# Kernel tuning notes

Measured on AMD Instinct MI355X. Metric: run time of the kernel, lower is better.

Reference implementation:

```python
import jax, jax.numpy as jnp
import numpy as np

B, N, DIN, DOUT = 2048, 64, 512, 512


def setup_inputs() -> dict:
    key = jax.random.key(0)
    kx, kw, kb = jax.random.split(key, 3)
    x = jax.random.normal(kx, (B, N, DIN), dtype=jnp.float32)
    # stacked per-node Linear params (PyTorch Linear: y = x @ W.T + b)
    bound = 1.0 / np.sqrt(DIN)
    W = jax.random.uniform(kw, (N, DIN, DOUT), dtype=jnp.float32, minval=-bound, maxval=bound)
    b = jax.random.uniform(kb, (N, DOUT), dtype=jnp.float32, minval=-bound, maxval=bound)
    return {"x": x, "W": W, "b": b}


def reference(x, W, b):
    # per-node independent linear layers fused into one batched GEMM
    # x: [B, N, DIN], W: [N, DIN, DOUT], b: [N, DOUT]
    y = jnp.einsum('bni,nio->bno', x, W) + b  # [B, N, DOUT]
    # torch.cat along dim=1 of the per-node [B, DOUT] outputs == flatten node axis
    return y.reshape(x.shape[0], -1)  # [B, N*DOUT]
```

## Files before the change

### kernel.cpp

```cpp
#include <hip/hip_runtime.h>


#define NN 64
#define DIN 512
#define DOUT 512
#define BM 128
#define BN 128
#define BK 32
#define LDK 40
#define ROWSTRIDE (NN * DIN)
#define OUTSTRIDE (NN * DOUT)

typedef __bf16 bf16x8 __attribute__((ext_vector_type(8)));
typedef float f32x4 __attribute__((ext_vector_type(4)));

__device__ __forceinline__ unsigned int f2bf_bits(float f) {
    unsigned int u = __builtin_bit_cast(unsigned int, f);
    return (u + 0x7fffu + ((u >> 16) & 1u)) >> 16;
}

__device__ __forceinline__ unsigned short f2bf(float f) {
    return (unsigned short)f2bf_bits(f);
}

__device__ __forceinline__ unsigned int f2bf2(float a, float b) {
    return f2bf_bits(a) | (f2bf_bits(b) << 16);
}

__global__ void wt_transpose_kernel(const float* __restrict__ W,
                                    unsigned short* __restrict__ Wt) {
    __shared__ float tile[32][33];
    const int n  = blockIdx.z;
    const int i0 = blockIdx.x * 32;
    const int o0 = blockIdx.y * 32;
    const float* Wn = W + (size_t)n * DIN * DOUT;
    unsigned short* Wtn = Wt + (size_t)n * DIN * DOUT;
    const int tx = threadIdx.x, ty = threadIdx.y;
#pragma unroll
    for (int q = 0; q < 4; ++q)
        tile[ty + q * 8][tx] = Wn[(size_t)(i0 + ty + q * 8) * DOUT + (o0 + tx)];
    __syncthreads();
#pragma unroll
    for (int q = 0; q < 4; ++q)
        Wtn[(size_t)(o0 + ty + q * 8) * DIN + (i0 + tx)] = f2bf(tile[tx][ty + q * 8]);
}

__global__ __launch_bounds__(256) void node_gemm_kernel(
    const float* __restrict__ X, const unsigned short* __restrict__ Wt,
    const float* __restrict__ Bias, float* __restrict__ Out) {
    __shared__ unsigned short As[2][BM][LDK];
    __shared__ unsigned short Bs[2][BN][LDK];

    const int bid = blockIdx.x;
    const int swz = (bid & 7) * 512 + (bid >> 3);
    const int node  = swz >> 6;
    const int rem   = swz & 63;
    const int mtile = rem >> 2;
    const int ntile = rem & 3;
    const int brow = mtile * BM;
    const int bcol = ntile * BN;

    const int tid  = threadIdx.x;
    const int lane = tid & 63;
    const int wave = tid >> 6;
    const int wm = wave >> 1, wn = wave & 1;

    const float* Xb = X + (size_t)brow * ROWSTRIDE + node * DIN;
    const unsigned short* Wb = Wt + (size_t)node * DIN * DOUT + (size_t)bcol * DIN;

    const int a_r = tid >> 3, a_c = tid & 7;
    const int b_r = tid >> 2, b_c = tid & 3;

    const int aoff = (wm * 64 + (lane & 15)) * LDK + (lane >> 4) * 8;
    const int boff = (wn * 64 + (lane & 15)) * LDK + (lane >> 4) * 8;

    f32x4 acc[4][4] = {};

    float4 arg[4];
    int4   brg[2];

#pragma unroll
    for (int q = 0; q < 4; ++q)
        arg[q] = *reinterpret_cast<const float4*>(Xb + (size_t)(a_r + q * 32) * ROWSTRIDE + a_c * 4);
#pragma unroll
    for (int q = 0; q < 2; ++q)
        brg[q] = *reinterpret_cast<const int4*>(Wb + (b_r + q * 64) * DIN + b_c * 8);
#pragma unroll
    for (int q = 0; q < 4; ++q) {
        uint2 p;
        p.x = f2bf2(arg[q].x, arg[q].y);
        p.y = f2bf2(arg[q].z, arg[q].w);
        *reinterpret_cast<uint2*>(&As[0][a_r + q * 32][a_c * 4]) = p;
    }
#pragma unroll
    for (int q = 0; q < 2; ++q)
        *reinterpret_cast<int4*>(&Bs[0][b_r + q * 64][b_c * 8]) = brg[q];
    __syncthreads();

    int cur = 0;
    for (int kt = 0; kt < DIN / BK; ++kt) {
        const int k0n = (kt + 1) * BK;
        const bool more = (kt < DIN / BK - 1);
        if (more) {
#pragma unroll
            for (int q = 0; q < 4; ++q)
                arg[q] = *reinterpret_cast<const float4*>(
                    Xb + (size_t)(a_r + q * 32) * ROWSTRIDE + k0n + a_c * 4);
#pragma unroll
            for (int q = 0; q < 2; ++q)
                brg[q] = *reinterpret_cast<const int4*>(Wb + (b_r + q * 64) * DIN + k0n + b_c * 8);
        }

        const unsigned short* Abase = &As[cur][0][0];
        const unsigned short* Bbase = &Bs[cur][0][0];
        bf16x8 af[4], bq[4];
#pragma unroll
        for (int m = 0; m < 4; ++m)
            af[m] = *reinterpret_cast<const bf16x8*>(Abase + aoff + m * 16 * LDK);
#pragma unroll
        for (int n = 0; n < 4; ++n)
            bq[n] = *reinterpret_cast<const bf16x8*>(Bbase + boff + n * 16 * LDK);
#pragma unroll
        for (int m = 0; m < 4; ++m)
#pragma unroll
            for (int n = 0; n < 4; ++n)
                acc[m][n] = __builtin_amdgcn_mfma_f32_16x16x32_bf16(af[m], bq[n], acc[m][n], 0, 0, 0);

        if (more) {
#pragma unroll
            for (int q = 0; q < 4; ++q) {
                uint2 p;
                p.x = f2bf2(arg[q].x, arg[q].y);
                p.y = f2bf2(arg[q].z, arg[q].w);
                *reinterpret_cast<uint2*>(&As[cur ^ 1][a_r + q * 32][a_c * 4]) = p;
            }
#pragma unroll
            for (int q = 0; q < 2; ++q)
                *reinterpret_cast<int4*>(&Bs[cur ^ 1][b_r + q * 64][b_c * 8]) = brg[q];
        }
        __syncthreads();
        cur ^= 1;
    }

    const float* bn = Bias + node * DOUT;
    float* outb = Out + (size_t)brow * OUTSTRIDE + node * DOUT;
#pragma unroll
    for (int n = 0; n < 4; ++n) {
        const int col = bcol + wn * 64 + n * 16 + (lane & 15);
        const float bias = bn[col];
#pragma unroll
        for (int m = 0; m < 4; ++m) {
            const int r0 = wm * 64 + m * 16 + ((lane >> 4) << 2);
#pragma unroll
            for (int j = 0; j < 4; ++j)
                outb[(size_t)(r0 + j) * OUTSTRIDE + col] = acc[m][n][j] + bias;
        }
    }
}

extern "C" void kernel_launch(void* const* d_in, const int* in_sizes, int n_in,
                              void* d_out, int out_size, void* d_ws, size_t ws_size,
                              hipStream_t stream) {
    const float* x = (const float*)d_in[0];
    const float* W = (const float*)d_in[1];
    const float* b = (const float*)d_in[2];
    float* out = (float*)d_out;
    unsigned short* Wt = (unsigned short*)d_ws;

    wt_transpose_kernel<<<dim3(DIN / 32, DOUT / 32, NN), dim3(32, 8), 0, stream>>>(W, Wt);
    node_gemm_kernel<<<dim3(4096), dim3(256), 0, stream>>>(x, Wt, b, out);
}
```

Measured before the change: 239.9 us.

## Use direct global-to-LDS loads for W with swizzled layout and 64x256 tiles

Reshapes the block tile from 128x128 to 64x256 so all four waves share the same A rows and each covers a 64-column slice of B. The bf16 weight tile is now moved straight into LDS with global_load_lds, using an XOR swizzle in place of padding, so it no longer goes through registers. Float-to-bf16 conversion of X uses the native cast. This cuts register pressure and VGPR traffic for B staging, but B reuse across the M tile drops and each block now reads more of W.

```diff
diff --git a/kernel.cpp b/kernel.cpp
--- a/kernel.cpp
+++ b/kernel.cpp
@@ -4,27 +4,28 @@
 #define NN 64
 #define DIN 512
 #define DOUT 512
-#define BM 128
-#define BN 128
+#define BM 64
+#define BN 256
 #define BK 32
 #define LDK 40
 #define ROWSTRIDE (NN * DIN)
 #define OUTSTRIDE (NN * DOUT)
+#define KSTEPS (DIN / BK)
 
 typedef __bf16 bf16x8 __attribute__((ext_vector_type(8)));
 typedef float f32x4 __attribute__((ext_vector_type(4)));
 
-__device__ __forceinline__ unsigned int f2bf_bits(float f) {
-    unsigned int u = __builtin_bit_cast(unsigned int, f);
-    return (u + 0x7fffu + ((u >> 16) & 1u)) >> 16;
+__device__ __forceinline__ unsigned short f2bf(float f) {
+    return __builtin_bit_cast(unsigned short, (__bf16)f);
+}
+__device__ __forceinline__ unsigned int f2bf2(float a, float b) {
+    return (unsigned int)f2bf(a) | ((unsigned int)f2bf(b) << 16);
 }
 
-__device__ __forceinline__ unsigned short f2bf(float f) {
-    return (unsigned short)f2bf_bits(f);
-}
-
-__device__ __forceinline__ unsigned int f2bf2(float a, float b) {
-    return f2bf_bits(a) | (f2bf_bits(b) << 16);
+typedef const __attribute__((address_space(1))) unsigned int* gas1_t;
+typedef __attribute__((address_space(3))) unsigned int* las3_t;
+__device__ __forceinline__ void gload_lds16(const void* g, void* l) {
+    __builtin_amdgcn_global_load_lds((gas1_t)g, (las3_t)l, 16, 0, 0);
 }
 
 __global__ void wt_transpose_kernel(const float* __restrict__ W,
@@ -48,109 +49,102 @@
 __global__ __launch_bounds__(256) void node_gemm_kernel(
     const float* __restrict__ X, const unsigned short* __restrict__ Wt,
     const float* __restrict__ Bias, float* __restrict__ Out) {
-    __shared__ unsigned short As[2][BM][LDK];
-    __shared__ unsigned short Bs[2][BN][LDK];
+    __shared__ unsigned short As[2][BM * LDK];
+    __shared__ unsigned short Bs[2][BN * BK];
 
     const int bid = blockIdx.x;
     const int swz = (bid & 7) * 512 + (bid >> 3);
     const int node  = swz >> 6;
     const int rem   = swz & 63;
-    const int mtile = rem >> 2;
-    const int ntile = rem & 3;
+    const int mtile = rem >> 1;
+    const int ntile = rem & 1;
     const int brow = mtile * BM;
     const int bcol = ntile * BN;
 
     const int tid  = threadIdx.x;
     const int lane = tid & 63;
-    const int wave = tid >> 6;
-    const int wm = wave >> 1, wn = wave & 1;
+    const int w    = tid >> 6;
 
     const float* Xb = X + (size_t)brow * ROWSTRIDE + node * DIN;
     const unsigned short* Wb = Wt + (size_t)node * DIN * DOUT + (size_t)bcol * DIN;
 
-    const int a_r = tid >> 3, a_c = tid & 7;
-    const int b_r = tid >> 2, b_c = tid & 3;
+    const int b_rl = lane >> 2;
+    const int b_cs = lane & 3;
 
-    const int aoff = (wm * 64 + (lane & 15)) * LDK + (lane >> 4) * 8;
-    const int boff = (wn * 64 + (lane & 15)) * LDK + (lane >> 4) * 8;
+    const int a_r = tid >> 2;
+    const int a_c = tid & 3;
+
+    const int arow = lane & 15;
+    const int akk  = lane >> 4;
+    const int aoff = arow * LDK + akk * 8;
+    const int obase = w * 64 + (lane & 15);
+    const int bswz  = akk ^ ((obase >> 1) & 3);
+    const int boff  = obase * BK + bswz * 8;
 
     f32x4 acc[4][4] = {};
+    float4 av0, av1;
 
-    float4 arg[4];
-    int4   brg[2];
+    auto stageB = [&](int buf, int k0) {
+#pragma unroll
+        for (int q = 0; q < 4; ++q) {
+            const int cb = q * 4 + w;
+            const int r  = cb * 16 + b_rl;
+            const int c  = b_cs ^ ((r >> 1) & 3);
+            gload_lds16(Wb + (size_t)r * DIN + k0 + c * 8, &Bs[buf][cb * 512]);
+        }
+    };
+    auto loadA = [&](int k0) {
+        const float* p = Xb + (size_t)a_r * ROWSTRIDE + k0 + a_c * 8;
+        av0 = *reinterpret_cast<const float4*>(p);
+        av1 = *reinterpret_cast<const float4*>(p + 4);
+    };
+    auto storeA = [&](int buf) {
+        uint4 pk;
+        pk.x = f2bf2(av0.x, av0.y);
+        pk.y = f2bf2(av0.z, av0.w);
+        pk.z = f2bf2(av1.x, av1.y);
+        pk.w = f2bf2(av1.z, av1.w);
+        *reinterpret_cast<uint4*>(&As[buf][a_r * LDK + a_c * 8]) = pk;
+    };
 
-#pragma unroll
-    for (int q = 0; q < 4; ++q)
-        arg[q] = *reinterpret_cast<const float4*>(Xb + (size_t)(a_r + q * 32) * ROWSTRIDE + a_c * 4);
-#pragma unroll
-    for (int q = 0; q < 2; ++q)
-        brg[q] = *reinterpret_cast<const int4*>(Wb + (b_r + q * 64) * DIN + b_c * 8);
-#pragma unroll
-    for (int q = 0; q < 4; ++q) {
-        uint2 p;
-        p.x = f2bf2(arg[q].x, arg[q].y);
-        p.y = f2bf2(arg[q].z, arg[q].w);
-        *reinterpret_cast<uint2*>(&As[0][a_r + q * 32][a_c * 4]) = p;
-    }
-#pragma unroll
-    for (int q = 0; q < 2; ++q)
-        *reinterpret_cast<int4*>(&Bs[0][b_r + q * 64][b_c * 8]) = brg[q];
+    loadA(0);
+    stageB(0, 0);
+    storeA(0);
     __syncthreads();
 
-    int cur = 0;
-    for (int kt = 0; kt < DIN / BK; ++kt) {
-        const int k0n = (kt + 1) * BK;
-        const bool more = (kt < DIN / BK - 1);
+    int buf = 0;
+    for (int kt = 0; kt < KSTEPS; ++kt) {
+        const bool more = (kt < KSTEPS - 1);
         if (more) {
-#pragma unroll
-            for (int q = 0; q < 4; ++q)
-                arg[q] = *reinterpret_cast<const float4*>(
-                    Xb + (size_t)(a_r + q * 32) * ROWSTRIDE + k0n + a_c * 4);
-#pragma unroll
-            for (int q = 0; q < 2; ++q)
-                brg[q] = *reinterpret_cast<const int4*>(Wb + (b_r + q * 64) * DIN + k0n + b_c * 8);
+            stageB(buf ^ 1, (kt + 1) * BK);
+            loadA((kt + 1) * BK);
         }
-
-        const unsigned short* Abase = &As[cur][0][0];
-        const unsigned short* Bbase = &Bs[cur][0][0];
         bf16x8 af[4], bq[4];
 #pragma unroll
         for (int m = 0; m < 4; ++m)
-            af[m] = *reinterpret_cast<const bf16x8*>(Abase + aoff + m * 16 * LDK);
+            af[m] = *reinterpret_cast<const bf16x8*>(&As[buf][aoff + m * 16 * LDK]);
 #pragma unroll
         for (int n = 0; n < 4; ++n)
-            bq[n] = *reinterpret_cast<const bf16x8*>(Bbase + boff + n * 16 * LDK);
+            bq[n] = *reinterpret_cast<const bf16x8*>(&Bs[buf][boff + n * 16 * BK]);
 #pragma unroll
         for (int m = 0; m < 4; ++m)
 #pragma unroll
             for (int n = 0; n < 4; ++n)
                 acc[m][n] = __builtin_amdgcn_mfma_f32_16x16x32_bf16(af[m], bq[n], acc[m][n], 0, 0, 0);
-
-        if (more) {
-#pragma unroll
-            for (int q = 0; q < 4; ++q) {
-                uint2 p;
-                p.x = f2bf2(arg[q].x, arg[q].y);
-                p.y = f2bf2(arg[q].z, arg[q].w);
-                *reinterpret_cast<uint2*>(&As[cur ^ 1][a_r + q * 32][a_c * 4]) = p;
-            }
-#pragma unroll
-            for (int q = 0; q < 2; ++q)
-                *reinterpret_cast<int4*>(&Bs[cur ^ 1][b_r + q * 64][b_c * 8]) = brg[q];
-        }
+        if (more) storeA(buf ^ 1);
         __syncthreads();
-        cur ^= 1;
+        buf ^= 1;
     }
 
-    const float* bn = Bias + node * DOUT;
-    float* outb = Out + (size_t)brow * OUTSTRIDE + node * DOUT;
+    const float* bn = Bias + node * DOUT + bcol;
+    float* outb = Out + (size_t)brow * OUTSTRIDE + node * DOUT + bcol;
 #pragma unroll
     for (int n = 0; n < 4; ++n) {
-        const int col = bcol + wn * 64 + n * 16 + (lane & 15);
+        const int col = w * 64 + n * 16 + (lane & 15);
         const float bias = bn[col];
 #pragma unroll
         for (int m = 0; m < 4; ++m) {
-            const int r0 = wm * 64 + m * 16 + ((lane >> 4) << 2);
+            const int r0 = m * 16 + akk * 4;
 #pragma unroll
             for (int j = 0; j < 4; ++j)
                 outb[(size_t)(r0 + j) * OUTSTRIDE + col] = acc[m][n][j] + bias;
```

After: 235.4 us. Within noise of the previous version (-1.9%).
